# Kernel tuning notes

Hardware: AMD Instinct MI355X
Metric: run time of the kernel (lower is better)

The kernel has to match this reference:

```python
import jax, jax.numpy as jnp
import numpy as np

B, N, D = 4, 2048, 1024
H, DH = 16, 64
INNER = H * DH
FF = 4 * D
EPS = 1e-5


def _layernorm(x, g, b):
    mu = jnp.mean(x, axis=-1, keepdims=True)
    var = jnp.var(x, axis=-1, keepdims=True)
    return (x - mu) * jax.lax.rsqrt(var + EPS) * g + b


def setup_inputs() -> dict:
    key = jax.random.key(0)
    ks = jax.random.split(key, 16)
    s = lambda i, shape, scale: jax.random.normal(ks[i], shape, dtype=jnp.float32) * scale
    return {
        "x": s(0, (B, N, D), 1.0),
        "ln1_g": jnp.ones((D,), jnp.float32),
        "ln1_b": jnp.zeros((D,), jnp.float32),
        "w_qkv": s(1, (D, 3 * INNER), D ** -0.5),
        "w_out": s(2, (INNER, D), INNER ** -0.5),
        "b_out": jnp.zeros((D,), jnp.float32),
        "ln2_g": jnp.ones((D,), jnp.float32),
        "ln2_b": jnp.zeros((D,), jnp.float32),
        "w_ff1": s(3, (D, FF), D ** -0.5),
        "b_ff1": jnp.zeros((FF,), jnp.float32),
        "w_ff2": s(4, (FF, D), FF ** -0.5),
        "b_ff2": jnp.zeros((D,), jnp.float32),
        "w_halt": s(5, (D, 1), D ** -0.5),
        "b_halt": jnp.zeros((1,), jnp.float32),
    }


def reference(x, ln1_g, ln1_b, w_qkv, w_out, b_out, ln2_g, ln2_b,
              w_ff1, b_ff1, w_ff2, b_ff2, w_halt, b_halt):
    scale = DH ** -0.5
    # --- PreNorm attention ---
    h = _layernorm(x, ln1_g, ln1_b)
    qkv = h @ w_qkv                      # [B, N, 3*INNER]
    q, k, v = jnp.split(qkv, 3, axis=-1)
    split_heads = lambda t: t.reshape(B, N, H, DH).transpose(0, 2, 1, 3)  # b h n d
    q, k, v = map(split_heads, (q, k, v))
    sim = jnp.einsum('bhid,bhjd->bhij', q, k) * scale  # [B,H,N,N]
    causal_mask = jnp.triu(jnp.ones((N, N), bool), k=1)
    sim = jnp.where(causal_mask, -jnp.finfo(sim.dtype).max, sim)
    attn = jax.nn.softmax(sim, axis=-1)
    out = jnp.einsum('bhij,bhjd->bhid', attn, v)
    out = out.transpose(0, 2, 1, 3).reshape(B, N, INNER)
    x = out @ w_out + b_out + x
    # --- PreNorm feedforward ---
    h = _layernorm(x, ln2_g, ln2_b)
    h = jax.nn.gelu(h @ w_ff1 + b_ff1, approximate=False) @ w_ff2 + b_ff2
    x = h + x
    # --- halt logits ---
    halt = (jnp.mean(x, axis=1) @ w_halt + b_halt)[:, 0]  # [B]
    return x, halt
```

## Files before the change

### kernel.cpp

```cpp
#include <hip/hip_runtime.h>
#include <stdint.h>


typedef unsigned short u16;
typedef __attribute__((ext_vector_type(8))) short short8v;
typedef __attribute__((ext_vector_type(4))) float f32x4;
typedef __attribute__((ext_vector_type(4))) u16 u16x4;

#define B_ 4
#define N_ 2048
#define D_ 1024
#define H_ 16
#define DH_ 64
#define ROWS_ (B_ * N_)

__device__ __forceinline__ u16 f2bf(float f) {
  union { float f; unsigned u; } v; v.f = f;
  unsigned r = v.u + 0x7fffu + ((v.u >> 16) & 1u);
  return (u16)(r >> 16);
}

__device__ __forceinline__ f32x4 mfma_b(short8v a, short8v b, f32x4 c) {
  asm volatile("v_mfma_f32_16x16x32_bf16 %0, %1, %2, %0" : "+v"(c) : "v"(a), "v"(b));
  return c;
}
__device__ __forceinline__ f32x4 mfma_b_vc(short8v a, short8v b, f32x4 c) {
  asm volatile("s_nop 1\n\tv_mfma_f32_16x16x32_bf16 %0, %1, %2, %0" : "+v"(c) : "v"(a), "v"(b));
  return c;
}
__device__ __forceinline__ f32x4 accfence(f32x4 v) {
  asm volatile("s_nop 7" : "+v"(v));
  return v;
}

__device__ __forceinline__ void async16(const void* g, void* l) {
  __builtin_amdgcn_global_load_lds((__attribute__((address_space(1))) unsigned int*)g,
                                   (__attribute__((address_space(3))) unsigned int*)l,
                                   16, 0, 0);
}

#define SWZ8(row, chunk) ((((chunk) ^ ((row) & 7)) << 3))

__global__ __launch_bounds__(256) void ln_kernel(const float* __restrict__ x,
    const float* __restrict__ gam, const float* __restrict__ bet,
    u16* __restrict__ out) {
  const int row = blockIdx.x;
  const int t = threadIdx.x;
  const float4 v = ((const float4*)(x + (size_t)row * D_))[t];
  float s  = v.x + v.y + v.z + v.w;
  float ss = v.x*v.x + v.y*v.y + v.z*v.z + v.w*v.w;
#pragma unroll
  for (int o = 32; o >= 1; o >>= 1) { s += __shfl_xor(s, o); ss += __shfl_xor(ss, o); }
  __shared__ float red[8];
  const int w = t >> 6;
  if ((t & 63) == 0) { red[w] = s; red[4 + w] = ss; }
  __syncthreads();
  s  = red[0] + red[1] + red[2] + red[3];
  ss = red[4] + red[5] + red[6] + red[7];
  const float mean = s * (1.0f / D_);
  const float var  = ss * (1.0f / D_) - mean * mean;
  const float rstd = rsqrtf(var + 1e-5f);
  const float4 g4 = ((const float4*)gam)[t];
  const float4 b4 = ((const float4*)bet)[t];
  u16x4 o4;
  o4.x = f2bf((v.x - mean) * rstd * g4.x + b4.x);
  o4.y = f2bf((v.y - mean) * rstd * g4.y + b4.y);
  o4.z = f2bf((v.z - mean) * rstd * g4.z + b4.z);
  o4.w = f2bf((v.w - mean) * rstd * g4.w + b4.w);
  *(u16x4*)(out + (size_t)row * D_ + t * 4) = o4;
}

__global__ __launch_bounds__(256) void transpose_all(
    const float* __restrict__ wqkv, const float* __restrict__ wout,
    const float* __restrict__ wff1, const float* __restrict__ wff2,
    u16* __restrict__ wqkvT, u16* __restrict__ woutT,
    u16* __restrict__ wff1T, u16* __restrict__ wff2T) {
  __shared__ float tile[32][33];
  int id = blockIdx.x;
  const float* W; u16* WT; int K, N, nt, kt;
  if (id < 3072)      { W = wqkv; WT = wqkvT; K = 1024; N = 3072; nt = id % 96;  kt = id / 96; }
  else if (id < 4096) { id -= 3072; W = wout; WT = woutT; K = 1024; N = 1024; nt = id % 32;  kt = id / 32; }
  else if (id < 8192) { id -= 4096; W = wff1; WT = wff1T; K = 1024; N = 4096; nt = id % 128; kt = id / 128; }
  else                { id -= 8192; W = wff2; WT = wff2T; K = 4096; N = 1024; nt = id % 32;  kt = id / 32; }
  const int n0 = nt * 32, k0 = kt * 32;
  const int tx = threadIdx.x, ty = threadIdx.y;
#pragma unroll
  for (int i = 0; i < 4; ++i)
    tile[ty + i * 8][tx] = W[(size_t)(k0 + ty + i * 8) * N + n0 + tx];
  __syncthreads();
#pragma unroll
  for (int i = 0; i < 4; ++i)
    WT[(size_t)(n0 + ty + i * 8) * K + k0 + tx] = f2bf(tile[tx][ty + i * 8]);
}

__global__ __launch_bounds__(256) void transpose_v(const u16* __restrict__ qkv,
    u16* __restrict__ vt) {
  __shared__ u16 tile[32][33];
  const int bh = blockIdx.z;
  const int bb = bh >> 4, hh = bh & 15;
  const int n0 = blockIdx.x * 32, d0 = blockIdx.y * 32;
  const int tx = threadIdx.x, ty = threadIdx.y;
#pragma unroll
  for (int i = 0; i < 4; ++i)
    tile[ty + i * 8][tx] =
        qkv[(size_t)(bb * N_ + n0 + ty + i * 8) * 3072 + 2048 + hh * DH_ + d0 + tx];
  __syncthreads();
#pragma unroll
  for (int i = 0; i < 4; ++i)
    vt[((size_t)bh * DH_ + d0 + ty + i * 8) * N_ + n0 + tx] = tile[tx][ty + i * 8];
}

__global__ __launch_bounds__(256) void gemm_bt(
    const u16* __restrict__ A, const u16* __restrict__ BT,
    int N, int K, int mode,
    const float* __restrict__ bias, const float* __restrict__ res,
    float* __restrict__ outf, u16* __restrict__ outb) {
  __shared__ alignas(16) u16 As[128 * 64];
  __shared__ alignas(16) u16 Bs[128 * 64];
  const int t = threadIdx.x;
  const int lane = t & 63, w = t >> 6;
  const int wm = w >> 1, wn = w & 1;
  const int cc = lane & 15, quad = lane >> 4;
  const int m0 = blockIdx.y * 128, n0 = blockIdx.x * 128;

  const f32x4 fz = {0.f, 0.f, 0.f, 0.f};
  f32x4 acc[4][4];
#pragma unroll
  for (int i = 0; i < 4; ++i)
#pragma unroll
    for (int j = 0; j < 4; ++j) acc[i][j] = fz;

  const int off0 = t * 16;
  for (int k0 = 0; k0 < K; k0 += 64) {
#pragma unroll
    for (int r = 0; r < 4; ++r) {
      const int off = r * 4096 + off0;
      const int row = off >> 7;
      const int cl  = ((off >> 4) & 7) ^ (row & 7);
      async16(A  + (size_t)(m0 + row) * K + k0 + cl * 8, (char*)As + off);
      async16(BT + (size_t)(n0 + row) * K + k0 + cl * 8, (char*)Bs + off);
    }
    __syncthreads();
#pragma unroll
    for (int kk = 0; kk < 2; ++kk) {
      short8v a[4], b[4];
#pragma unroll
      for (int i = 0; i < 4; ++i)
        a[i] = *(const short8v*)(As + (wm * 64 + i * 16 + cc) * 64 +
                                 SWZ8(cc, kk * 4 + quad));
#pragma unroll
      for (int j = 0; j < 4; ++j)
        b[j] = *(const short8v*)(Bs + (wn * 64 + j * 16 + cc) * 64 +
                                 SWZ8(cc, kk * 4 + quad));
#pragma unroll
      for (int i = 0; i < 4; ++i)
#pragma unroll
        for (int j = 0; j < 4; ++j) acc[i][j] = mfma_b(a[i], b[j], acc[i][j]);
    }
    __syncthreads();
  }

#pragma unroll
  for (int i = 0; i < 4; ++i) {
    const int row = m0 + wm * 64 + i * 16 + quad * 4;
#pragma unroll
    for (int j = 0; j < 4; ++j) {
      const int col = n0 + wn * 64 + j * 16 + cc;
      f32x4 v = accfence(acc[i][j]);
#pragma unroll
      for (int r = 0; r < 4; ++r) {
        const size_t idx = (size_t)(row + r) * N + col;
        float val = v[r];
        if (mode == 0) {
          outb[idx] = f2bf(val);
        } else if (mode == 2) {
          val += bias[col];
          val = 0.5f * val * (1.0f + erff(val * 0.70710678118654752f));
          outb[idx] = f2bf(val);
        } else {
          outf[idx] = val + bias[col] + res[idx];
        }
      }
    }
  }
}

__global__ __launch_bounds__(256, 2) void attn_kernel(const u16* __restrict__ qkv,
    const u16* __restrict__ vt, u16* __restrict__ outp) {
  const int f  = blockIdx.x;
  const int p  = (f >> 3) & 7;
  const int g  = ((f >> 6) << 3) | (f & 7);
  const int hh = g & 15, bb = g >> 4;
  const int t = threadIdx.x, lane = t & 63, w = t >> 6;
  const int cc = lane & 15, quad = lane >> 4;

  __shared__ alignas(16) u16 Ks[2][64 * 64];
  __shared__ alignas(16) u16 Vs[2][64 * 64];
  __shared__ alignas(16) u16 Ps[4][16 * 64];

  const u16* kbase = qkv + (size_t)bb * N_ * 3072 + 1024 + hh * DH_;
  const u16* vbase = vt + ((size_t)(bb * H_ + hh)) * DH_ * N_;

  const int soff0 = t * 16;
#pragma unroll
  for (int r = 0; r < 2; ++r) {
    const int off = r * 4096 + soff0;
    const int row = off >> 7;
    const int cl  = ((off >> 4) & 7) ^ (row & 7);
    async16(kbase + (size_t)row * 3072 + cl * 8, (char*)Ks[0] + off);
    async16(vbase + (size_t)row * N_ + cl * 8,   (char*)Vs[0] + off);
  }

  const f32x4 fz = {0.f, 0.f, 0.f, 0.f};
  const float C1 = 0.18033688011112042f;
  const float C2 = -11.541560327111707f;

  int bufc = 0;
#pragma unroll
  for (int ci = 0; ci < 2; ++ci) {
    const int qc = ci ? 15 - p : p;
    const int q0 = qc * 128;
    const int ktmax = 2 * qc + 1;

    short8v qa[2][2];
#pragma unroll
    for (int s = 0; s < 2; ++s)
#pragma unroll
      for (int h = 0; h < 2; ++h)
        qa[s][h] = *(const short8v*)(qkv +
            (size_t)(bb * N_ + q0 + s * 64 + w * 16 + cc) * 3072 +
            hh * DH_ + h * 32 + quad * 8);

    f32x4 of[2][4];
    float rs[2][4];
#pragma unroll
    for (int s = 0; s < 2; ++s)
#pragma unroll
      for (int n = 0; n < 4; ++n) { of[s][n] = fz; rs[s][n] = 0.f; }

    for (int kt = 0; kt <= ktmax; ++kt) {
      const int k0 = kt * 64;
      const int cur = bufc & 1;
      __syncthreads();

      if ((kt < ktmax) | (ci == 0)) {
        const int k1 = (kt < ktmax) ? k0 + 64 : 0;
#pragma unroll
        for (int r = 0; r < 2; ++r) {
          const int off = r * 4096 + soff0;
          const int row = off >> 7;
          const int cl  = ((off >> 4) & 7) ^ (row & 7);
          async16(kbase + (size_t)(k1 + row) * 3072 + cl * 8, (char*)Ks[cur ^ 1] + off);
          async16(vbase + (size_t)row * N_ + k1 + cl * 8,     (char*)Vs[cur ^ 1] + off);
        }
      }

      const u16* KsB = Ks[cur];
      const u16* VsB = Vs[cur];
      short8v kb[4][2], vb[4][2];
#pragma unroll
      for (int j = 0; j < 4; ++j)
#pragma unroll
        for (int h = 0; h < 2; ++h) {
          kb[j][h] = *(const short8v*)(KsB + (j * 16 + cc) * 64 + SWZ8(cc, h * 4 + quad));
          vb[j][h] = *(const short8v*)(VsB + (j * 16 + cc) * 64 + SWZ8(cc, h * 4 + quad));
        }

#pragma unroll
      for (int s = 0; s < 2; ++s) {
        const int Rbase = q0 + s * 64 + w * 16;
        if (k0 > Rbase + 15) continue;

        f32x4 sr[4];
#pragma unroll
        for (int j = 0; j < 4; ++j) {
          f32x4 z = fz;
          z = mfma_b_vc(qa[s][0], kb[j][0], z);
          z = mfma_b(qa[s][1], kb[j][1], z);
          sr[j] = accfence(z);
        }

        if (k0 + 63 > Rbase) {
#pragma unroll
          for (int j = 0; j < 4; ++j) {
            const int kcol = k0 + j * 16 + cc;
#pragma unroll
            for (int r = 0; r < 4; ++r) {
              float pv = __builtin_amdgcn_exp2f(fmaf(sr[j][r], C1, C2));
              pv = (kcol <= Rbase + quad * 4 + r) ? pv : 0.f;
              sr[j][r] = pv;
              rs[s][r] += pv;
            }
          }
        } else {
#pragma unroll
          for (int j = 0; j < 4; ++j)
#pragma unroll
            for (int r = 0; r < 4; ++r) {
              const float pv = __builtin_amdgcn_exp2f(fmaf(sr[j][r], C1, C2));
              sr[j][r] = pv;
              rs[s][r] += pv;
            }
        }

#pragma unroll
        for (int j = 0; j < 4; ++j)
#pragma unroll
          for (int r = 0; r < 4; ++r) {
            union { float f; unsigned u; } cv; cv.f = sr[j][r];
            const int rho = quad * 4 + r;
            const int Lc  = j * 2 + (cc >> 3);
            Ps[w][rho * 64 + (((Lc ^ (rho & 7)) << 3) | (cc & 7))] =
                (u16)((cv.u + 0x8000u) >> 16);
          }
        const short8v pa0 = *(const short8v*)(&Ps[w][cc * 64 + SWZ8(cc, quad)]);
        const short8v pa1 = *(const short8v*)(&Ps[w][cc * 64 + SWZ8(cc, 4 + quad)]);
#pragma unroll
        for (int n = 0; n < 4; ++n) {
          of[s][n] = mfma_b(pa0, vb[n][0], of[s][n]);
          of[s][n] = mfma_b(pa1, vb[n][1], of[s][n]);
        }
      }
      ++bufc;
    }

#pragma unroll
    for (int o = 1; o < 16; o <<= 1)
#pragma unroll
      for (int s = 0; s < 2; ++s)
#pragma unroll
        for (int r = 0; r < 4; ++r) rs[s][r] += __shfl_xor(rs[s][r], o);

#pragma unroll
    for (int s = 0; s < 2; ++s) {
      float inv[4];
#pragma unroll
      for (int r = 0; r < 4; ++r) inv[r] = 1.0f / rs[s][r];
#pragma unroll
      for (int n = 0; n < 4; ++n) {
        f32x4 o = accfence(of[s][n]);
#pragma unroll
        for (int r = 0; r < 4; ++r) {
          const size_t row = (size_t)(bb * N_ + q0 + s * 64 + w * 16 + quad * 4 + r);
          outp[row * 1024 + hh * DH_ + n * 16 + cc] = f2bf(o[r] * inv[r]);
        }
      }
    }
  }
}

__global__ void halt_init(float* __restrict__ hout, const float* __restrict__ bh) {
  if (threadIdx.x < B_) hout[threadIdx.x] = bh[0];
}

__global__ __launch_bounds__(256) void halt_partial(const float* __restrict__ xf,
    const float* __restrict__ wh, float* __restrict__ hout) {
  const int bb = blockIdx.y, sl = blockIdx.x;
  const size_t base = ((size_t)bb * N_ + sl * 64) * D_;
  float p = 0.f;
  for (int e = threadIdx.x; e < 64 * D_; e += 256)
    p += xf[base + e] * wh[e & (D_ - 1)];
#pragma unroll
  for (int o = 32; o >= 1; o >>= 1) p += __shfl_xor(p, o);
  __shared__ float red[4];
  const int w = threadIdx.x >> 6;
  if ((threadIdx.x & 63) == 0) red[w] = p;
  __syncthreads();
  if (threadIdx.x == 0)
    atomicAdd(&hout[bb], (red[0] + red[1] + red[2] + red[3]) * (1.0f / N_));
}

extern "C" void kernel_launch(void* const* d_in, const int* in_sizes, int n_in,
                              void* d_out, int out_size, void* d_ws, size_t ws_size,
                              hipStream_t stream) {
  (void)in_sizes; (void)n_in; (void)out_size; (void)ws_size;
  const float* x      = (const float*)d_in[0];
  const float* ln1_g  = (const float*)d_in[1];
  const float* ln1_b  = (const float*)d_in[2];
  const float* w_qkv  = (const float*)d_in[3];
  const float* w_out  = (const float*)d_in[4];
  const float* b_out  = (const float*)d_in[5];
  const float* ln2_g  = (const float*)d_in[6];
  const float* ln2_b  = (const float*)d_in[7];
  const float* w_ff1  = (const float*)d_in[8];
  const float* b_ff1  = (const float*)d_in[9];
  const float* w_ff2  = (const float*)d_in[10];
  const float* b_ff2  = (const float*)d_in[11];
  const float* w_halt = (const float*)d_in[12];
  const float* b_halt = (const float*)d_in[13];

  float* out_x    = (float*)d_out;
  float* out_halt = out_x + (size_t)ROWS_ * D_;

  char* ws = (char*)d_ws;
  u16* wqkvT = (u16*)(ws + 0);
  u16* woutT = (u16*)(ws + 6291456);
  u16* wff1T = (u16*)(ws + 8388608);
  u16* wff2T = (u16*)(ws + 16777216);
  char* RB   = ws + 25165824;
  u16* qkvb  = (u16*)(RB);
  u16* h1    = (u16*)(RB + 50331648);
  u16* attno = h1;
  u16* vtb   = (u16*)(RB + 67108864);
  u16* h2    = (u16*)(RB);
  u16* ff1b  = (u16*)(RB + 16777216);

  const dim3 tb(32, 8);
  transpose_all<<<12288, tb, 0, stream>>>(w_qkv, w_out, w_ff1, w_ff2,
                                          wqkvT, woutT, wff1T, wff2T);
  ln_kernel<<<ROWS_, 256, 0, stream>>>(x, ln1_g, ln1_b, h1);
  gemm_bt<<<dim3(24, 64), 256, 0, stream>>>(h1, wqkvT, 3072, 1024, 0,
                                            nullptr, nullptr, nullptr, qkvb);
  transpose_v<<<dim3(64, 2, 64), tb, 0, stream>>>(qkvb, vtb);
  attn_kernel<<<dim3(512), 256, 0, stream>>>(qkvb, vtb, attno);
  gemm_bt<<<dim3(8, 64), 256, 0, stream>>>(attno, woutT, 1024, 1024, 1,
                                           b_out, x, out_x, nullptr);
  ln_kernel<<<ROWS_, 256, 0, stream>>>(out_x, ln2_g, ln2_b, h2);
  gemm_bt<<<dim3(32, 64), 256, 0, stream>>>(h2, wff1T, 4096, 1024, 2,
                                            b_ff1, nullptr, nullptr, ff1b);
  gemm_bt<<<dim3(8, 64), 256, 0, stream>>>(ff1b, wff2T, 1024, 4096, 3,
                                           b_ff2, out_x, out_x, nullptr);
  halt_init<<<1, 64, 0, stream>>>(out_halt, b_halt);
  halt_partial<<<dim3(32, 4), 256, 0, stream>>>(out_x, w_halt, out_halt);
}
```

Baseline: 588.1 us.

## Remap GEMM blocks per XCD for L2 locality and use tanh-form GELU

Replaces the 2D GEMM grid with a 1D grid whose block index is decomposed so each of the 8 XCDs works on a contiguous rectangular region of output tiles, improving L2 reuse of A and B panels. The FF1 epilogue's erf-based GELU is replaced by the tanh approximation computed via exp2 and reciprocal intrinsics, cutting epilogue ALU cost. The approximation slightly changes numerics versus exact GELU, and the mapping assumes grid sizes divide evenly.

```diff
diff --git a/kernel.cpp b/kernel.cpp
--- a/kernel.cpp
+++ b/kernel.cpp
@@ -112,7 +112,7 @@
 
 __global__ __launch_bounds__(256) void gemm_bt(
     const u16* __restrict__ A, const u16* __restrict__ BT,
-    int N, int K, int mode,
+    int N, int K, int mode, int gx, int rw,
     const float* __restrict__ bias, const float* __restrict__ res,
     float* __restrict__ outf, u16* __restrict__ outb) {
   __shared__ alignas(16) u16 As[128 * 64];
@@ -121,14 +121,23 @@
   const int lane = t & 63, w = t >> 6;
   const int wm = w >> 1, wn = w & 1;
   const int cc = lane & 15, quad = lane >> 4;
-  const int m0 = blockIdx.y * 128, n0 = blockIdx.x * 128;
+
+  const int i   = blockIdx.x;
+  const int xcd = i & 7;
+  const int s   = i >> 3;
+  const int rcols = gx / rw;
+  const int rh  = (gridDim.x >> 3) / rw;
+  const int rcol = xcd % rcols, rrow = xcd / rcols;
+  const int lx = s % rw, ly = s / rw;
+  const int n0 = (rcol * rw + lx) * 128;
+  const int m0 = (rrow * rh + ly) * 128;
 
   const f32x4 fz = {0.f, 0.f, 0.f, 0.f};
   f32x4 acc[4][4];
 #pragma unroll
-  for (int i = 0; i < 4; ++i)
-#pragma unroll
-    for (int j = 0; j < 4; ++j) acc[i][j] = fz;
+  for (int i2 = 0; i2 < 4; ++i2)
+#pragma unroll
+    for (int j = 0; j < 4; ++j) acc[i2][j] = fz;
 
   const int off0 = t * 16;
   for (int k0 = 0; k0 < K; k0 += 64) {
@@ -145,28 +154,28 @@
     for (int kk = 0; kk < 2; ++kk) {
       short8v a[4], b[4];
 #pragma unroll
-      for (int i = 0; i < 4; ++i)
-        a[i] = *(const short8v*)(As + (wm * 64 + i * 16 + cc) * 64 +
-                                 SWZ8(cc, kk * 4 + quad));
+      for (int i2 = 0; i2 < 4; ++i2)
+        a[i2] = *(const short8v*)(As + (wm * 64 + i2 * 16 + cc) * 64 +
+                                  SWZ8(cc, kk * 4 + quad));
 #pragma unroll
       for (int j = 0; j < 4; ++j)
         b[j] = *(const short8v*)(Bs + (wn * 64 + j * 16 + cc) * 64 +
                                  SWZ8(cc, kk * 4 + quad));
 #pragma unroll
-      for (int i = 0; i < 4; ++i)
-#pragma unroll
-        for (int j = 0; j < 4; ++j) acc[i][j] = mfma_b(a[i], b[j], acc[i][j]);
+      for (int i2 = 0; i2 < 4; ++i2)
+#pragma unroll
+        for (int j = 0; j < 4; ++j) acc[i2][j] = mfma_b(a[i2], b[j], acc[i2][j]);
     }
     __syncthreads();
   }
 
 #pragma unroll
-  for (int i = 0; i < 4; ++i) {
-    const int row = m0 + wm * 64 + i * 16 + quad * 4;
+  for (int i2 = 0; i2 < 4; ++i2) {
+    const int row = m0 + wm * 64 + i2 * 16 + quad * 4;
 #pragma unroll
     for (int j = 0; j < 4; ++j) {
       const int col = n0 + wn * 64 + j * 16 + cc;
-      f32x4 v = accfence(acc[i][j]);
+      f32x4 v = accfence(acc[i2][j]);
 #pragma unroll
       for (int r = 0; r < 4; ++r) {
         const size_t idx = (size_t)(row + r) * N + col;
@@ -175,7 +184,9 @@
           outb[idx] = f2bf(val);
         } else if (mode == 2) {
           val += bias[col];
-          val = 0.5f * val * (1.0f + erff(val * 0.70710678118654752f));
+          const float zz = val * fmaf(val * val, 0.044715f, 1.0f);
+          const float e = __builtin_amdgcn_exp2f(-2.3022082f * zz);
+          val = val * __builtin_amdgcn_rcpf(1.0f + e);
           outb[idx] = f2bf(val);
         } else {
           outf[idx] = val + bias[col] + res[idx];
@@ -409,17 +420,17 @@
   transpose_all<<<12288, tb, 0, stream>>>(w_qkv, w_out, w_ff1, w_ff2,
                                           wqkvT, woutT, wff1T, wff2T);
   ln_kernel<<<ROWS_, 256, 0, stream>>>(x, ln1_g, ln1_b, h1);
-  gemm_bt<<<dim3(24, 64), 256, 0, stream>>>(h1, wqkvT, 3072, 1024, 0,
-                                            nullptr, nullptr, nullptr, qkvb);
+  gemm_bt<<<1536, 256, 0, stream>>>(h1, wqkvT, 3072, 1024, 0, 24, 12,
+                                    nullptr, nullptr, nullptr, qkvb);
   transpose_v<<<dim3(64, 2, 64), tb, 0, stream>>>(qkvb, vtb);
   attn_kernel<<<dim3(512), 256, 0, stream>>>(qkvb, vtb, attno);
-  gemm_bt<<<dim3(8, 64), 256, 0, stream>>>(attno, woutT, 1024, 1024, 1,
-                                           b_out, x, out_x, nullptr);
+  gemm_bt<<<512, 256, 0, stream>>>(attno, woutT, 1024, 1024, 1, 8, 8,
+                                   b_out, x, out_x, nullptr);
   ln_kernel<<<ROWS_, 256, 0, stream>>>(out_x, ln2_g, ln2_b, h2);
-  gemm_bt<<<dim3(32, 64), 256, 0, stream>>>(h2, wff1T, 4096, 1024, 2,
-                                            b_ff1, nullptr, nullptr, ff1b);
-  gemm_bt<<<dim3(8, 64), 256, 0, stream>>>(ff1b, wff2T, 1024, 4096, 3,
-                                           b_ff2, out_x, out_x, nullptr);
+  gemm_bt<<<2048, 256, 0, stream>>>(h2, wff1T, 4096, 1024, 2, 32, 16,
+                                    b_ff1, nullptr, nullptr, ff1b);
+  gemm_bt<<<512, 256, 0, stream>>>(ff1b, wff2T, 1024, 4096, 3, 8, 8,
+                                   b_ff2, out_x, out_x, nullptr);
   halt_init<<<1, 64, 0, stream>>>(out_halt, b_halt);
   halt_partial<<<dim3(32, 4), 256, 0, stream>>>(out_x, w_halt, out_halt);
 }
```

Measured after the change: 560.1 us. -4.8%, faster.
